# Performance work log

Hardware: AMD Instinct MI355X
Metric: run time of the kernel (lower is better)

Reference implementation:

```python
import jax, jax.numpy as jnp
import numpy as np

INPUT, HIDDEN = 100, 64
B, T = 1024, 512


def setup_inputs() -> dict:
    key = jax.random.key(0)
    ks = jax.random.split(key, 12)
    s_in = 1.0 / np.sqrt(HIDDEN)
    def u(k, shape):
        return jax.random.uniform(k, shape, jnp.float32, -s_in, s_in)
    return {
        "x": jax.random.normal(ks[0], (B, T, INPUT), jnp.float32),
        # layer 0 (PyTorch gate order: i, f, g, o stacked along first axis)
        "W_ih0": u(ks[1], (4 * HIDDEN, INPUT)),
        "W_hh0": u(ks[2], (4 * HIDDEN, HIDDEN)),
        "b_ih0": u(ks[3], (4 * HIDDEN,)),
        "b_hh0": u(ks[4], (4 * HIDDEN,)),
        # layer 1
        "W_ih1": u(ks[5], (4 * HIDDEN, HIDDEN)),
        "W_hh1": u(ks[6], (4 * HIDDEN, HIDDEN)),
        "b_ih1": u(ks[7], (4 * HIDDEN,)),
        "b_hh1": u(ks[8], (4 * HIDDEN,)),
        # final projection 64 -> 1
        "fc_w": u(ks[9], (1, HIDDEN)),
        "fc_b": u(ks[10], (1,)),
    }


def _lstm_layer(x, W_ih, W_hh, b_ih, b_hh):
    """x: [B, T, D] -> hidden sequence [B, T, H]. PyTorch LSTM cell math."""
    b, t, _ = x.shape
    h4 = W_hh.shape[0]
    H = h4 // 4
    # precompute input contribution for all timesteps: [T, B, 4H]
    xg = (jnp.einsum('btd,gd->btg', x, W_ih) + b_ih + b_hh).transpose(1, 0, 2)
    Whh_T = W_hh.T  # [H, 4H]

    def step(carry, xt):
        h, c = carry
        g = xt + h @ Whh_T  # [B, 4H]
        i, f, gg, o = jnp.split(g, 4, axis=-1)
        i = jax.nn.sigmoid(i)
        f = jax.nn.sigmoid(f)
        gg = jnp.tanh(gg)
        o = jax.nn.sigmoid(o)
        c = f * c + i * gg
        h = o * jnp.tanh(c)
        return (h, c), h

    h0 = jnp.zeros((b, H), x.dtype)
    c0 = jnp.zeros((b, H), x.dtype)
    _, hs = jax.lax.scan(step, (h0, c0), xg)  # hs: [T, B, H]
    return hs.transpose(1, 0, 2)


def reference(x, W_ih0, W_hh0, b_ih0, b_hh0, W_ih1, W_hh1, b_ih1, b_hh1, fc_w, fc_b):
    h = _lstm_layer(x, W_ih0, W_hh0, b_ih0, b_hh0)
    h = _lstm_layer(h, W_ih1, W_hh1, b_ih1, b_hh1)
    return h @ fc_w.T + fc_b  # [B, T, 1]
```

## Files before the change

### kernel.cpp

```cpp
#include <hip/hip_runtime.h>
#include <cstddef>

#define INPUT_D 100
#define HID 64
#define H4 256
#define BATCH 1024
#define SEQT 512
#define TC 8
#define NCHUNK (SEQT / TC)
#define BB 2
#define NB (BATCH / BB)

__device__ __forceinline__ float sigm(float x) {
    return __builtin_amdgcn_rcpf(1.0f + __expf(-x));
}
__device__ __forceinline__ float tanh_f(float x) {
    float e = __expf(2.0f * x);
    return 1.0f - 2.0f * __builtin_amdgcn_rcpf(e + 1.0f);
}

__global__ __launch_bounds__(256, 2) void lstm2_fused(
    const float* __restrict__ x,
    const float* __restrict__ Wih0, const float* __restrict__ Whh0,
    const float* __restrict__ bih0, const float* __restrict__ bhh0,
    const float* __restrict__ Wih1, const float* __restrict__ Whh1,
    const float* __restrict__ bih1, const float* __restrict__ bhh1,
    const float* __restrict__ fcw, const float* __restrict__ fcb,
    float* __restrict__ y)
{
    __shared__ __align__(16) float xs[BB][TC * INPUT_D];
    __shared__ float xg[TC][BB][H4];
    __shared__ __align__(16) float h0s[HID][BB];
    __shared__ __align__(16) float h1s[HID][BB];
    __shared__ float gbuf[4][BB][HID];
    __shared__ float ybuf[TC][BB];

    const int tid = threadIdx.x;
    const int u = tid & 63;
    const int r = tid;
    const int bbase = blockIdx.x * BB;

    float whh0r[HID], wih1r[HID], whh1r[HID];
    #pragma unroll
    for (int k = 0; k < HID; k += 4) {
        *(float4*)(whh0r + k) = *(const float4*)(Whh0 + (size_t)r * HID + k);
        *(float4*)(wih1r + k) = *(const float4*)(Wih1 + (size_t)r * HID + k);
        *(float4*)(whh1r + k) = *(const float4*)(Whh1 + (size_t)r * HID + k);
    }
    const float bias0 = bih0[r] + bhh0[r];
    const float bias1 = bih1[r] + bhh1[r];
    const float fw = fcw[u];
    const float fb = fcb[0];

    float c0[BB], c1[BB];
    #pragma unroll
    for (int b = 0; b < BB; ++b) { c0[b] = 0.f; c1[b] = 0.f; }
    if (tid < HID) {
        #pragma unroll
        for (int b = 0; b < BB; ++b) { h0s[tid][b] = 0.f; h1s[tid][b] = 0.f; }
    }

    for (int ch = 0; ch < NCHUNK; ++ch) {
        const int t0 = ch * TC;

        #pragma unroll
        for (int b = 0; b < BB; ++b) {
            const float* xp = x + ((size_t)(bbase + b) * SEQT + t0) * INPUT_D;
            for (int i = tid; i < TC * INPUT_D; i += 256) xs[b][i] = xp[i];
        }
        __syncthreads();

        float acc[BB][TC];
        #pragma unroll
        for (int b = 0; b < BB; ++b)
            #pragma unroll
            for (int t = 0; t < TC; ++t) acc[b][t] = bias0;

        const float* wrow = Wih0 + (size_t)r * INPUT_D;
        #pragma unroll 5
        for (int kq = 0; kq < INPUT_D / 4; ++kq) {
            const float4 w = *(const float4*)(wrow + kq * 4);
            #pragma unroll
            for (int b = 0; b < BB; ++b)
                #pragma unroll
                for (int t = 0; t < TC; ++t) {
                    const float4 xv = *(const float4*)(&xs[b][t * INPUT_D + kq * 4]);
                    float a = acc[b][t];
                    a = fmaf(w.x, xv.x, a);
                    a = fmaf(w.y, xv.y, a);
                    a = fmaf(w.z, xv.z, a);
                    a = fmaf(w.w, xv.w, a);
                    acc[b][t] = a;
                }
        }
        #pragma unroll
        for (int b = 0; b < BB; ++b)
            #pragma unroll
            for (int t = 0; t < TC; ++t) xg[t][b][r] = acc[b][t];
        __syncthreads();

        for (int tc = 0; tc < TC; ++tc) {
            float a0[BB];
            #pragma unroll
            for (int b = 0; b < BB; ++b) a0[b] = xg[tc][b][r];
            #pragma unroll
            for (int k = 0; k < HID; k += 2) {
                const float4 h = *(const float4*)(&h0s[k][0]);
                a0[0] = fmaf(whh0r[k],     h.x, a0[0]);
                a0[1] = fmaf(whh0r[k],     h.y, a0[1]);
                a0[0] = fmaf(whh0r[k + 1], h.z, a0[0]);
                a0[1] = fmaf(whh0r[k + 1], h.w, a0[1]);
            }
            {
                const int g = tid >> 6;
                #pragma unroll
                for (int b = 0; b < BB; ++b) gbuf[g][b][u] = a0[b];
            }
            __syncthreads();

            if (tid < HID) {
                float hv[BB];
                #pragma unroll
                for (int b = 0; b < BB; ++b) {
                    const float gi = gbuf[0][b][u];
                    const float gf = gbuf[1][b][u];
                    const float gg = gbuf[2][b][u];
                    const float go = gbuf[3][b][u];
                    const float iv = sigm(gi), fv = sigm(gf);
                    const float cv = tanh_f(gg), ov = sigm(go);
                    c0[b] = fmaf(fv, c0[b], iv * cv);
                    hv[b] = ov * tanh_f(c0[b]);
                }
                *(float2*)(&h0s[u][0]) = make_float2(hv[0], hv[1]);
            }
            __syncthreads();

            float a1[BB];
            #pragma unroll
            for (int b = 0; b < BB; ++b) a1[b] = bias1;
            #pragma unroll
            for (int k = 0; k < HID; k += 2) {
                const float4 hx = *(const float4*)(&h0s[k][0]);
                const float4 hp = *(const float4*)(&h1s[k][0]);
                a1[0] = fmaf(wih1r[k],     hx.x, a1[0]);
                a1[1] = fmaf(wih1r[k],     hx.y, a1[1]);
                a1[0] = fmaf(wih1r[k + 1], hx.z, a1[0]);
                a1[1] = fmaf(wih1r[k + 1], hx.w, a1[1]);
                a1[0] = fmaf(whh1r[k],     hp.x, a1[0]);
                a1[1] = fmaf(whh1r[k],     hp.y, a1[1]);
                a1[0] = fmaf(whh1r[k + 1], hp.z, a1[0]);
                a1[1] = fmaf(whh1r[k + 1], hp.w, a1[1]);
            }
            {
                const int g = tid >> 6;
                #pragma unroll
                for (int b = 0; b < BB; ++b) gbuf[g][b][u] = a1[b];
            }
            __syncthreads();

            if (tid < HID) {
                float hv[BB], p[BB];
                #pragma unroll
                for (int b = 0; b < BB; ++b) {
                    const float gi = gbuf[0][b][u];
                    const float gf = gbuf[1][b][u];
                    const float gg = gbuf[2][b][u];
                    const float go = gbuf[3][b][u];
                    const float iv = sigm(gi), fv = sigm(gf);
                    const float cv = tanh_f(gg), ov = sigm(go);
                    c1[b] = fmaf(fv, c1[b], iv * cv);
                    hv[b] = ov * tanh_f(c1[b]);
                    p[b] = fw * hv[b];
                }
                *(float2*)(&h1s[u][0]) = make_float2(hv[0], hv[1]);
                #pragma unroll
                for (int off = 32; off >= 1; off >>= 1) {
                    #pragma unroll
                    for (int b = 0; b < BB; ++b) p[b] += __shfl_xor(p[b], off, 64);
                }
                if (u == 0) {
                    #pragma unroll
                    for (int b = 0; b < BB; ++b) ybuf[tc][b] = p[b] + fb;
                }
            }
            __syncthreads();
        }

        if (tid < TC * BB) {
            const int b = tid / TC;
            const int t = tid % TC;
            y[(size_t)(bbase + b) * SEQT + t0 + t] = ybuf[t][b];
        }
    }
}

extern "C" void kernel_launch(void* const* d_in, const int* in_sizes, int n_in,
                              void* d_out, int out_size, void* d_ws, size_t ws_size,
                              hipStream_t stream) {
    const float* x    = (const float*)d_in[0];
    const float* Wih0 = (const float*)d_in[1];
    const float* Whh0 = (const float*)d_in[2];
    const float* bih0 = (const float*)d_in[3];
    const float* bhh0 = (const float*)d_in[4];
    const float* Wih1 = (const float*)d_in[5];
    const float* Whh1 = (const float*)d_in[6];
    const float* bih1 = (const float*)d_in[7];
    const float* bhh1 = (const float*)d_in[8];
    const float* fcw  = (const float*)d_in[9];
    const float* fcb  = (const float*)d_in[10];
    float* y = (float*)d_out;

    lstm2_fused<<<NB, 256, 0, stream>>>(x, Wih0, Whh0, bih0, bhh0,
                                        Wih1, Whh1, bih1, bhh1, fcw, fcb, y);
}
```

Measured before the change: 2.553 ms.

## Split K across waves with 512 threads and readlane broadcasts for recurrent matvecs

Doubles the block to 512 threads. Each pair of waves splits the 64-wide hidden dot products in half, and partial sums are combined in shared-memory buffers. Hidden-state values are broadcast with readlane instead of LDS float4 reads, and the layer-1 recurrent term for the next step is computed right after h1 is produced, so the per-timestep critical path has fewer dependent matvecs. Gate math now runs on 128 threads, one per (unit, batch) pair, instead of 64 threads each looping over the batch. The cost is more partial-sum LDS traffic and doubled register pressure per block under launch_bounds(512,2).

```diff
diff --git a/kernel.cpp b/kernel.cpp
--- a/kernel.cpp
+++ b/kernel.cpp
@@ -3,7 +3,6 @@
 
 #define INPUT_D 100
 #define HID 64
-#define H4 256
 #define BATCH 1024
 #define SEQT 512
 #define TC 8
@@ -18,8 +17,11 @@
     float e = __expf(2.0f * x);
     return 1.0f - 2.0f * __builtin_amdgcn_rcpf(e + 1.0f);
 }
-
-__global__ __launch_bounds__(256, 2) void lstm2_fused(
+__device__ __forceinline__ float bcast(int v, int l) {
+    return __int_as_float(__builtin_amdgcn_readlane(v, l));
+}
+
+__global__ __launch_bounds__(512, 2) void lstm2_fused(
     const float* __restrict__ x,
     const float* __restrict__ Wih0, const float* __restrict__ Whh0,
     const float* __restrict__ bih0, const float* __restrict__ bhh0,
@@ -29,167 +31,167 @@
     float* __restrict__ y)
 {
     __shared__ __align__(16) float xs[BB][TC * INPUT_D];
-    __shared__ float xg[TC][BB][H4];
-    __shared__ __align__(16) float h0s[HID][BB];
-    __shared__ __align__(16) float h1s[HID][BB];
-    __shared__ float gbuf[4][BB][HID];
+    __shared__ float xg[TC][BB][256];
+    __shared__ __align__(8) float h0s[HID][BB];
+    __shared__ __align__(8) float h1s[HID][BB];
+    __shared__ __align__(8) float pb_L0[2][256][BB];
+    __shared__ __align__(8) float pb_L1[2][256][BB];
+    __shared__ __align__(8) float pb_W1[2][256][BB];
     __shared__ float ybuf[TC][BB];
 
-    const int tid = threadIdx.x;
-    const int u = tid & 63;
-    const int r = tid;
+    const int t    = threadIdx.x;
+    const int lane = t & 63;
+    const int wv   = t >> 6;
+    const int kh   = wv & 1;
+    const int q    = wv >> 1;
+    const int r    = q * 64 + lane;
+    const int khBase = __builtin_amdgcn_readfirstlane(kh * 32);
     const int bbase = blockIdx.x * BB;
 
-    float whh0r[HID], wih1r[HID], whh1r[HID];
-    #pragma unroll
-    for (int k = 0; k < HID; k += 4) {
-        *(float4*)(whh0r + k) = *(const float4*)(Whh0 + (size_t)r * HID + k);
-        *(float4*)(wih1r + k) = *(const float4*)(Wih1 + (size_t)r * HID + k);
-        *(float4*)(whh1r + k) = *(const float4*)(Whh1 + (size_t)r * HID + k);
+    float w0h[32], w1i[32], w1h[32];
+    {
+        const size_t o = (size_t)r * HID + kh * 32;
+        #pragma unroll
+        for (int kk = 0; kk < 32; kk += 4) {
+            *(float4*)(w0h + kk) = *(const float4*)(Whh0 + o + kk);
+            *(float4*)(w1i + kk) = *(const float4*)(Wih1 + o + kk);
+            *(float4*)(w1h + kk) = *(const float4*)(Whh1 + o + kk);
+        }
     }
-    const float bias0 = bih0[r] + bhh0[r];
-    const float bias1 = bih1[r] + bhh1[r];
-    const float fw = fcw[u];
+    const float bias1B = (kh == 0) ? (bih1[r] + bhh1[r]) : 0.0f;
+
+    const int p  = t & 127;
+    const int cg = t >> 7;
+    const float b0a = bih0[p] + bhh0[p];
+    const float b0b = bih0[p + 128] + bhh0[p + 128];
+
+    const int uu = t & 63;
+    const int ub = (t >> 6) & 1;
+    float c0 = 0.f, c1 = 0.f;
+    const float fw = fcw[uu];
     const float fb = fcb[0];
 
-    float c0[BB], c1[BB];
-    #pragma unroll
-    for (int b = 0; b < BB; ++b) { c0[b] = 0.f; c1[b] = 0.f; }
-    if (tid < HID) {
-        #pragma unroll
-        for (int b = 0; b < BB; ++b) { h0s[tid][b] = 0.f; h1s[tid][b] = 0.f; }
-    }
+    *(float2*)&pb_L0[kh][r][0] = make_float2(0.f, 0.f);
+    *(float2*)&pb_W1[kh][r][0] = make_float2(bias1B, bias1B);
 
     for (int ch = 0; ch < NCHUNK; ++ch) {
-        const int t0 = ch * TC;
-
-        #pragma unroll
-        for (int b = 0; b < BB; ++b) {
-            const float* xp = x + ((size_t)(bbase + b) * SEQT + t0) * INPUT_D;
-            for (int i = tid; i < TC * INPUT_D; i += 256) xs[b][i] = xp[i];
+        if (t < 400) {
+            const int e = t * 4;
+            const int b = (e >= TC * INPUT_D) ? 1 : 0;
+            const int off = e - b * (TC * INPUT_D);
+            const float4 v = *(const float4*)(
+                x + ((size_t)(bbase + b) * SEQT + (size_t)ch * TC) * INPUT_D + off);
+            *(float4*)&xs[b][off] = v;
         }
         __syncthreads();
 
-        float acc[BB][TC];
-        #pragma unroll
-        for (int b = 0; b < BB; ++b)
+        {
+            float acc0[4], acc1[4];
             #pragma unroll
-            for (int t = 0; t < TC; ++t) acc[b][t] = bias0;
-
-        const float* wrow = Wih0 + (size_t)r * INPUT_D;
-        #pragma unroll 5
-        for (int kq = 0; kq < INPUT_D / 4; ++kq) {
-            const float4 w = *(const float4*)(wrow + kq * 4);
+            for (int j = 0; j < 4; ++j) { acc0[j] = b0a; acc1[j] = b0b; }
+            const float* wa = Wih0 + (size_t)p * INPUT_D;
+            const float* wb = Wih0 + (size_t)(p + 128) * INPUT_D;
+            #pragma unroll 5
+            for (int kq = 0; kq < INPUT_D / 4; ++kq) {
+                const float4 va = *(const float4*)(wa + kq * 4);
+                const float4 vb = *(const float4*)(wb + kq * 4);
+                #pragma unroll
+                for (int j = 0; j < 4; ++j) {
+                    const int c  = cg * 4 + j;
+                    const int tc = c >> 1, b = c & 1;
+                    const float4 xv = *(const float4*)(&xs[b][tc * INPUT_D + kq * 4]);
+                    acc0[j] = fmaf(va.x, xv.x, acc0[j]);
+                    acc0[j] = fmaf(va.y, xv.y, acc0[j]);
+                    acc0[j] = fmaf(va.z, xv.z, acc0[j]);
+                    acc0[j] = fmaf(va.w, xv.w, acc0[j]);
+                    acc1[j] = fmaf(vb.x, xv.x, acc1[j]);
+                    acc1[j] = fmaf(vb.y, xv.y, acc1[j]);
+                    acc1[j] = fmaf(vb.z, xv.z, acc1[j]);
+                    acc1[j] = fmaf(vb.w, xv.w, acc1[j]);
+                }
+            }
             #pragma unroll
-            for (int b = 0; b < BB; ++b)
-                #pragma unroll
-                for (int t = 0; t < TC; ++t) {
-                    const float4 xv = *(const float4*)(&xs[b][t * INPUT_D + kq * 4]);
-                    float a = acc[b][t];
-                    a = fmaf(w.x, xv.x, a);
-                    a = fmaf(w.y, xv.y, a);
-                    a = fmaf(w.z, xv.z, a);
-                    a = fmaf(w.w, xv.w, a);
-                    acc[b][t] = a;
-                }
-        }
-        #pragma unroll
-        for (int b = 0; b < BB; ++b)
-            #pragma unroll
-            for (int t = 0; t < TC; ++t) xg[t][b][r] = acc[b][t];
+            for (int j = 0; j < 4; ++j) {
+                const int c = cg * 4 + j;
+                const int tc = c >> 1, b = c & 1;
+                xg[tc][b][p]       = acc0[j];
+                xg[tc][b][p + 128] = acc1[j];
+            }
+        }
         __syncthreads();
 
         for (int tc = 0; tc < TC; ++tc) {
-            float a0[BB];
-            #pragma unroll
-            for (int b = 0; b < BB; ++b) a0[b] = xg[tc][b][r];
-            #pragma unroll
-            for (int k = 0; k < HID; k += 2) {
-                const float4 h = *(const float4*)(&h0s[k][0]);
-                a0[0] = fmaf(whh0r[k],     h.x, a0[0]);
-                a0[1] = fmaf(whh0r[k],     h.y, a0[1]);
-                a0[0] = fmaf(whh0r[k + 1], h.z, a0[0]);
-                a0[1] = fmaf(whh0r[k + 1], h.w, a0[1]);
-            }
+            if (t < 128) {
+                float sv[4];
+                #pragma unroll
+                for (int g = 0; g < 4; ++g) {
+                    const int rg = g * 64 + uu;
+                    sv[g] = pb_L0[0][rg][ub] + pb_L0[1][rg][ub] + xg[tc][ub][rg];
+                }
+                const float iv = sigm(sv[0]), fv = sigm(sv[1]);
+                const float gv = tanh_f(sv[2]), ov = sigm(sv[3]);
+                c0 = fmaf(fv, c0, iv * gv);
+                h0s[uu][ub] = ov * tanh_f(c0);
+            }
+            __syncthreads();
+
             {
-                const int g = tid >> 6;
-                #pragma unroll
-                for (int b = 0; b < BB; ++b) gbuf[g][b][u] = a0[b];
-            }
-            __syncthreads();
-
-            if (tid < HID) {
-                float hv[BB];
-                #pragma unroll
-                for (int b = 0; b < BB; ++b) {
-                    const float gi = gbuf[0][b][u];
-                    const float gf = gbuf[1][b][u];
-                    const float gg = gbuf[2][b][u];
-                    const float go = gbuf[3][b][u];
-                    const float iv = sigm(gi), fv = sigm(gf);
-                    const float cv = tanh_f(gg), ov = sigm(go);
-                    c0[b] = fmaf(fv, c0[b], iv * cv);
-                    hv[b] = ov * tanh_f(c0[b]);
-                }
-                *(float2*)(&h0s[u][0]) = make_float2(hv[0], hv[1]);
-            }
-            __syncthreads();
-
-            float a1[BB];
-            #pragma unroll
-            for (int b = 0; b < BB; ++b) a1[b] = bias1;
-            #pragma unroll
-            for (int k = 0; k < HID; k += 2) {
-                const float4 hx = *(const float4*)(&h0s[k][0]);
-                const float4 hp = *(const float4*)(&h1s[k][0]);
-                a1[0] = fmaf(wih1r[k],     hx.x, a1[0]);
-                a1[1] = fmaf(wih1r[k],     hx.y, a1[1]);
-                a1[0] = fmaf(wih1r[k + 1], hx.z, a1[0]);
-                a1[1] = fmaf(wih1r[k + 1], hx.w, a1[1]);
-                a1[0] = fmaf(whh1r[k],     hp.x, a1[0]);
-                a1[1] = fmaf(whh1r[k],     hp.y, a1[1]);
-                a1[0] = fmaf(whh1r[k + 1], hp.z, a1[0]);
-                a1[1] = fmaf(whh1r[k + 1], hp.w, a1[1]);
-            }
+                const float2 hv = *(const float2*)&h0s[lane][0];
+                const int hb0 = __float_as_int(hv.x), hb1 = __float_as_int(hv.y);
+                float aL0b0 = 0.f, aL0b1 = 0.f, aL1b0 = 0.f, aL1b1 = 0.f;
+                #pragma unroll
+                for (int kk = 0; kk < 32; ++kk) {
+                    const float x0 = bcast(hb0, khBase + kk);
+                    const float x1 = bcast(hb1, khBase + kk);
+                    aL0b0 = fmaf(w0h[kk], x0, aL0b0);
+                    aL0b1 = fmaf(w0h[kk], x1, aL0b1);
+                    aL1b0 = fmaf(w1i[kk], x0, aL1b0);
+                    aL1b1 = fmaf(w1i[kk], x1, aL1b1);
+                }
+                *(float2*)&pb_L0[kh][r][0] = make_float2(aL0b0, aL0b1);
+                *(float2*)&pb_L1[kh][r][0] = make_float2(aL1b0, aL1b1);
+            }
+            __syncthreads();
+
+            if (t < 128) {
+                float sv[4];
+                #pragma unroll
+                for (int g = 0; g < 4; ++g) {
+                    const int rg = g * 64 + uu;
+                    sv[g] = pb_L1[0][rg][ub] + pb_L1[1][rg][ub]
+                          + pb_W1[0][rg][ub] + pb_W1[1][rg][ub];
+                }
+                const float iv = sigm(sv[0]), fv = sigm(sv[1]);
+                const float gv = tanh_f(sv[2]), ov = sigm(sv[3]);
+                c1 = fmaf(fv, c1, iv * gv);
+                const float h = ov * tanh_f(c1);
+                h1s[uu][ub] = h;
+                float pr = fw * h;
+                #pragma unroll
+                for (int off = 32; off >= 1; off >>= 1) pr += __shfl_xor(pr, off, 64);
+                if (uu == 0) ybuf[tc][ub] = pr + fb;
+            }
+            __syncthreads();
+
             {
-                const int g = tid >> 6;
-                #pragma unroll
-                for (int b = 0; b < BB; ++b) gbuf[g][b][u] = a1[b];
-            }
-            __syncthreads();
-
-            if (tid < HID) {
-                float hv[BB], p[BB];
-                #pragma unroll
-                for (int b = 0; b < BB; ++b) {
-                    const float gi = gbuf[0][b][u];
-                    const float gf = gbuf[1][b][u];
-                    const float gg = gbuf[2][b][u];
-                    const float go = gbuf[3][b][u];
-                    const float iv = sigm(gi), fv = sigm(gf);
-                    const float cv = tanh_f(gg), ov = sigm(go);
-                    c1[b] = fmaf(fv, c1[b], iv * cv);
-                    hv[b] = ov * tanh_f(c1[b]);
-                    p[b] = fw * hv[b];
-                }
-                *(float2*)(&h1s[u][0]) = make_float2(hv[0], hv[1]);
-                #pragma unroll
-                for (int off = 32; off >= 1; off >>= 1) {
-                    #pragma unroll
-                    for (int b = 0; b < BB; ++b) p[b] += __shfl_xor(p[b], off, 64);
-                }
-                if (u == 0) {
-                    #pragma unroll
-                    for (int b = 0; b < BB; ++b) ybuf[tc][b] = p[b] + fb;
-                }
-            }
-            __syncthreads();
-        }
-
-        if (tid < TC * BB) {
-            const int b = tid / TC;
-            const int t = tid % TC;
-            y[(size_t)(bbase + b) * SEQT + t0 + t] = ybuf[t][b];
+                const float2 hv = *(const float2*)&h1s[lane][0];
+                const int hb0 = __float_as_int(hv.x), hb1 = __float_as_int(hv.y);
+                float aWb0 = bias1B, aWb1 = bias1B;
+                #pragma unroll
+                for (int kk = 0; kk < 32; ++kk) {
+                    const float x0 = bcast(hb0, khBase + kk);
+                    const float x1 = bcast(hb1, khBase + kk);
+                    aWb0 = fmaf(w1h[kk], x0, aWb0);
+                    aWb1 = fmaf(w1h[kk], x1, aWb1);
+                }
+                *(float2*)&pb_W1[kh][r][0] = make_float2(aWb0, aWb1);
+            }
+            __syncthreads();
+        }
+
+        if (t < TC * BB) {
+            const int b = t / TC, tt = t % TC;
+            y[(size_t)(bbase + b) * SEQT + (size_t)ch * TC + tt] = ybuf[tt][b];
         }
     }
 }
@@ -210,6 +212,6 @@
     const float* fcb  = (const float*)d_in[10];
     float* y = (float*)d_out;
 
-    lstm2_fused<<<NB, 256, 0, stream>>>(x, Wih0, Whh0, bih0, bhh0,
+    lstm2_fused<<<NB, 512, 0, stream>>>(x, Wih0, Whh0, bih0, bhh0,
                                         Wih1, Whh1, bih1, bhh1, fcw, fcb, y);
 }
```

After: 3.820 ms. 1.5x slower.
